# Kernel tuning notes

Hardware: AMD Instinct MI355X
Metric: run time of the kernel (lower is better)

The kernel has to match this reference:

```python
import jax, jax.numpy as jnp
import numpy as np

B, V, N, F = 8, 4, 4096, 256
DV, DA = 64, 128
SF = DV + DA          # slot_full_size = 192
Q = 128               # qry_size
S = 7                 # num_slots
HID = 256             # residual MLP hidden
NUM_STEPS = 3
COEF = 1.0 / np.sqrt(Q).astype(np.float32)
EPS = 1e-5


def _ln(x, g, b):
    m = x.mean(-1, keepdims=True)
    v = ((x - m) ** 2).mean(-1, keepdims=True)
    return (x - m) / jnp.sqrt(v + EPS) * g + b


def _gru(u, h, Wi, Wh, bi, bh):
    gi = u @ Wi + bi
    gh = h @ Wh + bh
    ir, iz, inn = jnp.split(gi, 3, axis=-1)
    hr, hz, hn = jnp.split(gh, 3, axis=-1)
    r = jax.nn.sigmoid(ir + hr)
    z = jax.nn.sigmoid(iz + hz)
    nn_ = jnp.tanh(inn + r * hn)
    return (1.0 - z) * nn_ + z * h


def setup_inputs() -> dict:
    key = jax.random.key(0)
    ks = jax.random.split(key, 12)
    r = lambda k, sh: jax.random.normal(k, sh, jnp.float32) * 0.05
    return {
        'x': jax.random.normal(ks[0], (B, V, N, F), jnp.float32),
        'noise_view': jax.random.normal(ks[1], (B, V, DV), jnp.float32),
        'noise_obj_attr': jax.random.normal(ks[2], (B, S - 1, DA), jnp.float32),
        'noise_bck_attr': jax.random.normal(ks[3], (B, 1, DA), jnp.float32),
        'ln_in_g': jnp.ones((F,), jnp.float32), 'ln_in_b': jnp.zeros((F,), jnp.float32),
        'ln_qry_g': jnp.ones((SF,), jnp.float32), 'ln_qry_b': jnp.zeros((SF,), jnp.float32),
        'ln_res_g': jnp.ones((SF,), jnp.float32), 'ln_res_b': jnp.zeros((SF,), jnp.float32),
        'view_loc': jnp.zeros((DV,), jnp.float32), 'view_log_scl': jnp.zeros((DV,), jnp.float32),
        'attr_obj_loc': jnp.zeros((DA,), jnp.float32), 'attr_obj_scl': jnp.zeros((DA,), jnp.float32),
        'attr_bck_loc': jnp.zeros((DA,), jnp.float32), 'attr_bck_scl': jnp.zeros((DA,), jnp.float32),
        'W_qry': r(ks[4], (SF, Q)), 'W_key': r(ks[5], (F, Q)), 'W_val': r(ks[6], (F, SF)),
        'gru_Wi': r(ks[7], (SF, 3 * SF)), 'gru_Wh': r(ks[8], (SF, 3 * SF)),
        'gru_bi': jnp.zeros((3 * SF,), jnp.float32), 'gru_bh': jnp.zeros((3 * SF,), jnp.float32),
        'mlp_W1': r(ks[9], (SF, HID)), 'mlp_b1': jnp.zeros((HID,), jnp.float32),
        'mlp_W2': r(ks[10], (HID, SF)), 'mlp_b2': jnp.zeros((SF,), jnp.float32),
        'num_slots': S,
    }


def reference(x, noise_view, noise_obj_attr, noise_bck_attr,
              ln_in_g, ln_in_b, ln_qry_g, ln_qry_b, ln_res_g, ln_res_b,
              view_loc, view_log_scl, attr_obj_loc, attr_obj_scl, attr_bck_loc, attr_bck_scl,
              W_qry, W_key, W_val, gru_Wi, gru_Wh, gru_bi, gru_bh,
              mlp_W1, mlp_b1, mlp_W2, mlp_b2, num_slots):
    b, v = x.shape[:2]
    xl = _ln(x, ln_in_g, ln_in_b)
    x_key = xl @ W_key   # [b,v,n,Q]
    x_val = xl @ W_val   # [b,v,n,SF]
    slots_view = view_loc + jnp.exp(view_log_scl) * noise_view                      # [b,v,DV]
    slots_attr = jnp.concatenate([
        attr_obj_loc + jnp.exp(attr_obj_scl) * noise_obj_attr,
        attr_bck_loc + jnp.exp(attr_bck_scl) * noise_bck_attr], axis=1)             # [b,s,DA]
    s = num_slots
    for _ in range(NUM_STEPS):
        full = jnp.concatenate([
            jnp.broadcast_to(slots_view[:, :, None, :], (b, v, s, DV)),
            jnp.broadcast_to(slots_attr[:, None, :, :], (b, v, s, DA))], axis=-1)   # [b,v,s,SF]
        q = _ln(full, ln_qry_g, ln_qry_b) @ W_qry * COEF                            # [b,v,s,Q]
        logits = jnp.einsum('bvni,bvsi->bvns', x_key, q)
        logits = jax.nn.log_softmax(logits, axis=-1)   # over slots
        attn = jax.nn.softmax(logits, axis=-2)         # over inputs
        updates = jnp.einsum('bvns,bvni->bvsi', attn, x_val)                        # [b,v,s,SF]
        main = _gru(updates.reshape(-1, SF), full.reshape(-1, SF),
                    gru_Wi, gru_Wh, gru_bi, gru_bh).reshape(b, v, s, SF)
        res = jax.nn.relu(_ln(main, ln_res_g, ln_res_b) @ mlp_W1 + mlp_b1) @ mlp_W2 + mlp_b2
        full = main + res
        slots_view = full[..., :DV].mean(axis=2)   # mean over slots
        slots_attr = full[..., DV:].mean(axis=1)   # mean over views
    return slots_view, slots_attr
```

## Files before the change

kernel.cpp:

```cpp
#include <hip/hip_runtime.h>
#include <cstdint>
#include <cstddef>

typedef float  f32x4 __attribute__((ext_vector_type(4)));
typedef short  s16x8 __attribute__((ext_vector_type(8)));
typedef __bf16 bf16x8 __attribute__((ext_vector_type(8)));

static __device__ __forceinline__ f32x4 mfma16(s16x8 a, s16x8 b, f32x4 c) {
    return __builtin_amdgcn_mfma_f32_16x16x32_bf16(
        __builtin_bit_cast(bf16x8, a), __builtin_bit_cast(bf16x8, b), c, 0, 0, 0);
}

static __device__ __forceinline__ unsigned short f2bf(float f) {
    unsigned int u = __builtin_bit_cast(unsigned int, f);
    u = (u + 0x7fffu + ((u >> 16) & 1u)) >> 16;
    return (unsigned short)u;
}
static __device__ __forceinline__ float bf2f(unsigned short h) {
    unsigned int u = ((unsigned int)h) << 16;
    return __builtin_bit_cast(float, u);
}

#define COEF 0.08838834764831845f

__global__ __launch_bounds__(256) void k_prep(
    const float* __restrict__ Wkey, const float* __restrict__ Wval,
    const float* __restrict__ vloc, const float* __restrict__ vlscl, const float* __restrict__ nview,
    const float* __restrict__ aoloc, const float* __restrict__ aoscl, const float* __restrict__ nobj,
    const float* __restrict__ abloc, const float* __restrict__ abscl, const float* __restrict__ nbck,
    const float* __restrict__ Wi, const float* __restrict__ Wh,
    const float* __restrict__ W1, const float* __restrict__ W2,
    unsigned short* __restrict__ Wt, unsigned short* __restrict__ qbf,
    float* __restrict__ sview, float* __restrict__ sattr,
    unsigned short* __restrict__ Wib, unsigned short* __restrict__ Whb,
    unsigned short* __restrict__ W1b, unsigned short* __restrict__ W2b)
{
    int blk = blockIdx.x, t = threadIdx.x;
    if (blk < 320) {
        float v = (blk < 128) ? Wkey[t * 128 + blk] : Wval[t * 192 + (blk - 128)];
        Wt[blk * 256 + t] = f2bf(v);
    } else if (blk < 356) {
        int g = (blk - 320) * 256 + t;
        if (g < 2048) {
            int d = g & 63;
            sview[g] = vloc[d] + __expf(vlscl[d]) * nview[g];
        } else {
            int u = g - 2048;
            int b = u / 896, r = u % 896, s = r >> 7, d = r & 127;
            float val;
            if (s < 6) val = aoloc[d] + __expf(aoscl[d]) * nobj[(b * 6 + s) * 128 + d];
            else       val = abloc[d] + __expf(abscl[d]) * nbck[b * 128 + d];
            sattr[u] = val;
        }
    } else if (blk < 360) {
        for (int e = (blk - 356) * 256 + t; e < 32 * 9 * 128; e += 1024) {
            int bv = e / 1152, r = e % 1152, s = 7 + r / 128, k = r & 127;
            qbf[(bv * 16 + s) * 128 + k] = 0;
        }
    } else {
        const float* srcp; unsigned short* dstp; int g4;
        if (blk < 468)      { srcp = Wi; dstp = Wib; g4 = (blk - 360) * 256 + t; }
        else if (blk < 576) { srcp = Wh; dstp = Whb; g4 = (blk - 468) * 256 + t; }
        else if (blk < 624) { srcp = W1; dstp = W1b; g4 = (blk - 576) * 256 + t; }
        else                { srcp = W2; dstp = W2b; g4 = (blk - 624) * 256 + t; }
        float4 v = *(const float4*)(srcp + g4 * 4);
        unsigned u0 = (unsigned)f2bf(v.x) | ((unsigned)f2bf(v.y) << 16);
        unsigned u1 = (unsigned)f2bf(v.z) | ((unsigned)f2bf(v.w) << 16);
        *(uint2*)(dstp + g4 * 4) = make_uint2(u0, u1);
    }
}

__global__ __launch_bounds__(256) void k_lnkv(
    const float* __restrict__ x, const float* __restrict__ lng, const float* __restrict__ lnb,
    const unsigned short* __restrict__ Wt, unsigned short* __restrict__ xkv)
{
    __shared__ unsigned short lds[64 * 320];
    const int t = threadIdx.x, wave = t >> 6, lane = t & 63;
    const int l15 = lane & 15, lg = lane >> 4;
    const long rowbase = (long)blockIdx.x * 64;

    float4 gv = *(const float4*)(lng + lane * 4);
    float4 bv = *(const float4*)(lnb + lane * 4);
    for (int r = 0; r < 16; ++r) {
        int row = wave * 16 + r;
        float4 xv = *(const float4*)(x + (rowbase + row) * 256 + lane * 4);
        float s1 = xv.x + xv.y + xv.z + xv.w;
        float s2 = xv.x * xv.x + xv.y * xv.y + xv.z * xv.z + xv.w * xv.w;
        #pragma unroll
        for (int o = 32; o > 0; o >>= 1) { s1 += __shfl_xor(s1, o); s2 += __shfl_xor(s2, o); }
        float mean = s1 * (1.f / 256.f);
        float var  = s2 * (1.f / 256.f) - mean * mean;
        float rstd = rsqrtf(var + 1e-5f);
        float y0 = (xv.x - mean) * rstd * gv.x + bv.x;
        float y1 = (xv.y - mean) * rstd * gv.y + bv.y;
        float y2 = (xv.z - mean) * rstd * gv.z + bv.z;
        float y3 = (xv.w - mean) * rstd * gv.w + bv.w;
        unsigned int u0 = (unsigned)f2bf(y0) | ((unsigned)f2bf(y1) << 16);
        unsigned int u1 = (unsigned)f2bf(y2) | ((unsigned)f2bf(y3) << 16);
        int off = row * 512 + ((lane * 8) ^ ((row & 7) << 4));
        *(uint2*)((char*)lds + off) = make_uint2(u0, u1);
    }
    __syncthreads();

    f32x4 acc[4][5];
    #pragma unroll
    for (int mt = 0; mt < 4; ++mt)
        #pragma unroll
        for (int nt = 0; nt < 5; ++nt) acc[mt][nt] = (f32x4){0.f, 0.f, 0.f, 0.f};

    const int nb = wave * 80;
    #pragma unroll
    for (int kk = 0; kk < 8; ++kk) {
        s16x8 a[4], b[5];
        #pragma unroll
        for (int mt = 0; mt < 4; ++mt) {
            int row = mt * 16 + l15;
            int off = row * 512 + ((kk * 64 + lg * 16) ^ ((row & 7) << 4));
            a[mt] = *(const s16x8*)((char*)lds + off);
        }
        #pragma unroll
        for (int nt = 0; nt < 5; ++nt) {
            int col = nb + nt * 16 + l15;
            b[nt] = *(const s16x8*)(Wt + col * 256 + kk * 32 + lg * 8);
        }
        #pragma unroll
        for (int mt = 0; mt < 4; ++mt)
            #pragma unroll
            for (int nt = 0; nt < 5; ++nt)
                acc[mt][nt] = mfma16(a[mt], b[nt], acc[mt][nt]);
    }
    __syncthreads();

    #pragma unroll
    for (int mt = 0; mt < 4; ++mt)
        #pragma unroll
        for (int nt = 0; nt < 5; ++nt)
            #pragma unroll
            for (int rg = 0; rg < 4; ++rg) {
                int row = mt * 16 + lg * 4 + rg;
                int col = nb + nt * 16 + l15;
                lds[row * 320 + col] = f2bf(acc[mt][nt][rg]);
            }
    __syncthreads();
    const uint4* src = (const uint4*)lds;
    uint4* dst = (uint4*)(xkv + rowbase * 320);
    #pragma unroll
    for (int j = 0; j < 10; ++j) dst[j * 256 + t] = src[j * 256 + t];
}

__global__ __launch_bounds__(384) void k_qry(
    const float* __restrict__ sview, const float* __restrict__ sattr,
    const float* __restrict__ fnewp, int use_fnew,
    const float* __restrict__ lng, const float* __restrict__ lnb,
    const float* __restrict__ Wq, float* __restrict__ full, unsigned short* __restrict__ qbf)
{
    int row = blockIdx.x;
    int bv = row / 7, s = row % 7, b = bv >> 2;
    int j = threadIdx.x;
    __shared__ float fr[192];
    __shared__ float part[384];
    __shared__ float red[8];
    float v = 0.f;
    if (j < 192) {
        if (use_fnew) {
            if (j < 64) {
                float a = 0.f;
                #pragma unroll
                for (int sp = 0; sp < 7; ++sp) a += fnewp[(bv * 7 + sp) * 192 + j];
                v = a * (1.f / 7.f);
            } else {
                float a = 0.f;
                #pragma unroll
                for (int vv = 0; vv < 4; ++vv) a += fnewp[((b * 4 + vv) * 7 + s) * 192 + j];
                v = a * 0.25f;
            }
        } else {
            v = (j < 64) ? sview[bv * 64 + j] : sattr[(b * 7 + s) * 128 + (j - 64)];
        }
        full[row * 192 + j] = v;
        float s1 = v, s2 = v * v;
        #pragma unroll
        for (int o = 32; o > 0; o >>= 1) { s1 += __shfl_xor(s1, o); s2 += __shfl_xor(s2, o); }
        int wave = j >> 6, lane = j & 63;
        if (lane == 0) { red[wave] = s1; red[4 + wave] = s2; }
    }
    __syncthreads();
    if (j < 192) {
        float ts = red[0] + red[1] + red[2], ts2 = red[4] + red[5] + red[6];
        float mean = ts * (1.f / 192.f);
        float var  = ts2 * (1.f / 192.f) - mean * mean;
        float rstd = rsqrtf(var + 1e-5f);
        fr[j] = (v - mean) * rstd * lng[j] + lnb[j];
    }
    __syncthreads();
    {
        int c = j & 127, seg = j >> 7;
        float acc = 0.f;
        #pragma unroll
        for (int k = 0; k < 64; ++k) acc += fr[seg * 64 + k] * Wq[(seg * 64 + k) * 128 + c];
        part[j] = acc;
    }
    __syncthreads();
    if (j < 128) {
        float acc = part[j] + part[128 + j] + part[256 + j];
        qbf[(bv * 16 + s) * 128 + j] = f2bf(acc * COEF);
    }
}

__global__ __launch_bounds__(256) void k_attu(
    const unsigned short* __restrict__ qbf, const unsigned short* __restrict__ xkv,
    float* __restrict__ pU, float* __restrict__ pZ)
{
    int blk = blockIdx.x;
    int bv = blk >> 5, chunk = blk & 31;
    int n0 = chunk * 128;
    int t = threadIdx.x, wave = t >> 6, lane = t & 63;
    int l15 = lane & 15, lg = lane >> 4;
    __shared__ float wl[128 * 8];

    s16x8 aq[4];
    const unsigned short* qrow = qbf + (bv * 16 + l15) * 128 + lg * 8;
    #pragma unroll
    for (int kk = 0; kk < 4; ++kk) aq[kk] = *(const s16x8*)(qrow + kk * 32);

    #pragma unroll
    for (int batch = 0; batch < 2; ++batch) {
        int nloc = batch * 64 + wave * 16;
        const unsigned short* xr = xkv + ((long)(bv * 4096 + n0 + nloc + l15)) * 320 + lg * 8;
        f32x4 acc = (f32x4){0.f, 0.f, 0.f, 0.f};
        #pragma unroll
        for (int kk = 0; kk < 4; ++kk) {
            s16x8 bfr = *(const s16x8*)(xr + kk * 32);
            acc = mfma16(aq[kk], bfr, acc);
        }
        float o0 = __shfl_xor(acc[0], 16), o1 = __shfl_xor(acc[1], 16);
        float o2 = __shfl_xor(acc[2], 16), o3 = __shfl_xor(acc[3], 16);
        bool hi = (lg & 1);
        float v0 = hi ? o0 : acc[0], v1 = hi ? o1 : acc[1];
        float v2 = hi ? o2 : acc[2], v3 = hi ? o3 : acc[3];
        float v4 = hi ? acc[0] : o0, v5 = hi ? acc[1] : o1, v6 = hi ? acc[2] : o2;
        float m = fmaxf(fmaxf(fmaxf(v0, v1), fmaxf(v2, v3)), fmaxf(fmaxf(v4, v5), v6));
        float e0 = __expf(v0 - m), e1 = __expf(v1 - m), e2 = __expf(v2 - m), e3 = __expf(v3 - m);
        float e4 = __expf(v4 - m), e5 = __expf(v5 - m), e6 = __expf(v6 - m);
        float inv = 1.f / (e0 + e1 + e2 + e3 + e4 + e5 + e6);
        if (lg < 2) {
            int n = nloc + l15;
            float4 out = (lg == 0) ? make_float4(e0 * inv, e1 * inv, e2 * inv, e3 * inv)
                                   : make_float4(e4 * inv, e5 * inv, e6 * inv, 0.f);
            *(float4*)(wl + n * 8 + lg * 4) = out;
        }
    }
    __syncthreads();

    {
        f32x4 uacc[3];
        #pragma unroll
        for (int it = 0; it < 3; ++it) uacc[it] = (f32x4){0.f, 0.f, 0.f, 0.f};
        const unsigned short* vbase = xkv + ((long)(bv * 4096 + n0)) * 320 + 128;

        #pragma unroll
        for (int kb = 0; kb < 4; ++kb) {
            s16x8 aw = (s16x8){0, 0, 0, 0, 0, 0, 0, 0};
            if (l15 < 8) {
                #pragma unroll
                for (int j2 = 0; j2 < 8; ++j2)
                    aw[j2] = (short)f2bf(wl[(kb * 32 + lg * 8 + j2) * 8 + l15]);
            }
            #pragma unroll
            for (int it = 0; it < 3; ++it) {
                int col = wave * 48 + it * 16 + l15;
                s16x8 bw;
                #pragma unroll
                for (int j2 = 0; j2 < 8; ++j2)
                    bw[j2] = (short)vbase[(long)(kb * 32 + lg * 8 + j2) * 320 + col];
                uacc[it] = mfma16(aw, bw, uacc[it]);
            }
        }

        long base = (((long)bv * 32 + chunk) * 7) * 192;
        #pragma unroll
        for (int it = 0; it < 3; ++it) {
            int col = wave * 48 + it * 16 + l15;
            #pragma unroll
            for (int rg = 0; rg < 4; ++rg) {
                int s = lg * 4 + rg;
                if (s < 7) pU[base + s * 192 + col] = uacc[it][rg];
            }
        }
    }

    if (t < 112) {
        int s = t >> 4, part = t & 15;
        float z = 0.f;
        #pragma unroll
        for (int k = 0; k < 8; ++k) z += wl[(part + 16 * k) * 8 + s];
        #pragma unroll
        for (int o = 8; o > 0; o >>= 1) z += __shfl_xor(z, o);
        if (part == 0) pZ[(bv * 32 + chunk) * 7 + s] = z;
    }
}

__global__ __launch_bounds__(576) void k_gru(
    const float* __restrict__ pU, const float* __restrict__ pZ, const float* __restrict__ full,
    const unsigned short* __restrict__ Wib, const unsigned short* __restrict__ Whb,
    const float* __restrict__ bi, const float* __restrict__ bh,
    const float* __restrict__ lng, const float* __restrict__ lnb,
    const unsigned short* __restrict__ W1b, const float* __restrict__ b1,
    const unsigned short* __restrict__ W2b, const float* __restrict__ b2,
    float* __restrict__ fnew)
{
    int row = blockIdx.x;
    int bv = row / 7, s = row % 7;
    int j = threadIdx.x;
    __shared__ float u[192], h[192], gi[576], gh[576], lnm[192], h1[256], red[8];

    if (j < 192) {
        float u0 = 0.f, u1 = 0.f, u2 = 0.f, u3 = 0.f;
        #pragma unroll 4
        for (int c = 0; c < 32; c += 4) {
            u0 += pU[(((long)bv * 32 + c + 0) * 7 + s) * 192 + j];
            u1 += pU[(((long)bv * 32 + c + 1) * 7 + s) * 192 + j];
            u2 += pU[(((long)bv * 32 + c + 2) * 7 + s) * 192 + j];
            u3 += pU[(((long)bv * 32 + c + 3) * 7 + s) * 192 + j];
        }
        float z0 = 0.f, z1 = 0.f, z2 = 0.f, z3 = 0.f;
        #pragma unroll 4
        for (int c = 0; c < 32; c += 4) {
            z0 += pZ[(bv * 32 + c + 0) * 7 + s];
            z1 += pZ[(bv * 32 + c + 1) * 7 + s];
            z2 += pZ[(bv * 32 + c + 2) * 7 + s];
            z3 += pZ[(bv * 32 + c + 3) * 7 + s];
        }
        u[j] = ((u0 + u1) + (u2 + u3)) / ((z0 + z1) + (z2 + z3));
    } else if (j < 384) {
        int jj = j - 192;
        h[jj] = full[row * 192 + jj];
    }
    __syncthreads();

    {
        float a0 = 0.f, a1 = 0.f, a2 = 0.f, a3 = 0.f;
        float b0 = 0.f, b1v = 0.f, b2v = 0.f, b3 = 0.f;
        #pragma unroll 4
        for (int k = 0; k < 192; k += 4) {
            float uk0 = u[k], uk1 = u[k + 1], uk2 = u[k + 2], uk3 = u[k + 3];
            float hk0 = h[k], hk1 = h[k + 1], hk2 = h[k + 2], hk3 = h[k + 3];
            a0  += uk0 * bf2f(Wib[(k + 0) * 576 + j]);
            a1  += uk1 * bf2f(Wib[(k + 1) * 576 + j]);
            a2  += uk2 * bf2f(Wib[(k + 2) * 576 + j]);
            a3  += uk3 * bf2f(Wib[(k + 3) * 576 + j]);
            b0  += hk0 * bf2f(Whb[(k + 0) * 576 + j]);
            b1v += hk1 * bf2f(Whb[(k + 1) * 576 + j]);
            b2v += hk2 * bf2f(Whb[(k + 2) * 576 + j]);
            b3  += hk3 * bf2f(Whb[(k + 3) * 576 + j]);
        }
        gi[j] = ((a0 + a1) + (a2 + a3)) + bi[j];
        gh[j] = ((b0 + b1v) + (b2v + b3)) + bh[j];
    }
    __syncthreads();

    float mn = 0.f;
    if (j < 192) {
        float hv = h[j];
        float r  = 1.f / (1.f + __expf(-(gi[j] + gh[j])));
        float z  = 1.f / (1.f + __expf(-(gi[192 + j] + gh[192 + j])));
        float nn = tanhf(gi[384 + j] + r * gh[384 + j]);
        mn = (1.f - z) * nn + z * hv;

        float s1 = mn, s2 = mn * mn;
        #pragma unroll
        for (int o = 32; o > 0; o >>= 1) { s1 += __shfl_xor(s1, o); s2 += __shfl_xor(s2, o); }
        int wave = j >> 6, lane = j & 63;
        if (lane == 0) { red[wave] = s1; red[4 + wave] = s2; }
    }
    __syncthreads();
    if (j < 192) {
        float ts = red[0] + red[1] + red[2], ts2 = red[4] + red[5] + red[6];
        float mean = ts * (1.f / 192.f);
        float var  = ts2 * (1.f / 192.f) - mean * mean;
        float rstd = rsqrtf(var + 1e-5f);
        lnm[j] = (mn - mean) * rstd * lng[j] + lnb[j];
    }
    __syncthreads();

    if (j < 256) {
        float a0 = 0.f, a1 = 0.f, a2 = 0.f, a3 = 0.f;
        #pragma unroll 4
        for (int k = 0; k < 192; k += 4) {
            a0 += lnm[k + 0] * bf2f(W1b[(k + 0) * 256 + j]);
            a1 += lnm[k + 1] * bf2f(W1b[(k + 1) * 256 + j]);
            a2 += lnm[k + 2] * bf2f(W1b[(k + 2) * 256 + j]);
            a3 += lnm[k + 3] * bf2f(W1b[(k + 3) * 256 + j]);
        }
        h1[j] = fmaxf(((a0 + a1) + (a2 + a3)) + b1[j], 0.f);
    }
    __syncthreads();

    if (j < 192) {
        float a0 = 0.f, a1 = 0.f, a2 = 0.f, a3 = 0.f;
        #pragma unroll 4
        for (int c = 0; c < 256; c += 4) {
            a0 += h1[c + 0] * bf2f(W2b[(c + 0) * 192 + j]);
            a1 += h1[c + 1] * bf2f(W2b[(c + 1) * 192 + j]);
            a2 += h1[c + 2] * bf2f(W2b[(c + 2) * 192 + j]);
            a3 += h1[c + 3] * bf2f(W2b[(c + 3) * 192 + j]);
        }
        fnew[row * 192 + j] = mn + (((a0 + a1) + (a2 + a3)) + b2[j]);
    }
}

__global__ __launch_bounds__(256) void k_means(
    const float* __restrict__ fnew, float* __restrict__ oview, float* __restrict__ oattr)
{
    int t = blockIdx.x * 256 + threadIdx.x;
    if (t < 2048) {
        int bv = t >> 6, d = t & 63;
        float a = 0.f;
        #pragma unroll
        for (int s = 0; s < 7; ++s) a += fnew[(bv * 7 + s) * 192 + d];
        oview[t] = a * (1.f / 7.f);
    } else if (t < 9216) {
        int u = t - 2048;
        int b = u / 896, r = u % 896, s = r >> 7, d = r & 127;
        float a = 0.f;
        #pragma unroll
        for (int v = 0; v < 4; ++v) a += fnew[((b * 4 + v) * 7 + s) * 192 + 64 + d];
        oattr[u] = a * 0.25f;
    }
}

extern "C" void kernel_launch(void* const* d_in, const int* in_sizes, int n_in,
                              void* d_out, int out_size, void* d_ws, size_t ws_size,
                              hipStream_t stream)
{
    const float* x          = (const float*)d_in[0];
    const float* noise_view = (const float*)d_in[1];
    const float* noise_obj  = (const float*)d_in[2];
    const float* noise_bck  = (const float*)d_in[3];
    const float* ln_in_g    = (const float*)d_in[4];
    const float* ln_in_b    = (const float*)d_in[5];
    const float* ln_qry_g   = (const float*)d_in[6];
    const float* ln_qry_b   = (const float*)d_in[7];
    const float* ln_res_g   = (const float*)d_in[8];
    const float* ln_res_b   = (const float*)d_in[9];
    const float* view_loc   = (const float*)d_in[10];
    const float* view_lscl  = (const float*)d_in[11];
    const float* ao_loc     = (const float*)d_in[12];
    const float* ao_scl     = (const float*)d_in[13];
    const float* ab_loc     = (const float*)d_in[14];
    const float* ab_scl     = (const float*)d_in[15];
    const float* W_qry      = (const float*)d_in[16];
    const float* W_key      = (const float*)d_in[17];
    const float* W_val      = (const float*)d_in[18];
    const float* gru_Wi     = (const float*)d_in[19];
    const float* gru_Wh     = (const float*)d_in[20];
    const float* gru_bi     = (const float*)d_in[21];
    const float* gru_bh     = (const float*)d_in[22];
    const float* mlp_W1     = (const float*)d_in[23];
    const float* mlp_b1     = (const float*)d_in[24];
    const float* mlp_W2     = (const float*)d_in[25];
    const float* mlp_b2     = (const float*)d_in[26];

    char* ws = (char*)d_ws;
    size_t off = 0;
    auto alloc = [&](size_t bytes) { void* p = ws + off; off += (bytes + 255) & ~255ULL; return p; };
    unsigned short* xkv = (unsigned short*)alloc(131072UL * 320 * 2);
    unsigned short* Wt  = (unsigned short*)alloc(320UL * 256 * 2);
    unsigned short* qbf = (unsigned short*)alloc(32UL * 16 * 128 * 2);
    float* pU    = (float*)alloc(32UL * 32 * 7 * 192 * 4);
    float* pZ    = (float*)alloc(32UL * 32 * 7 * 4);
    float* fullb = (float*)alloc(224UL * 192 * 4);
    float* fnew  = (float*)alloc(224UL * 192 * 4);
    float* sview = (float*)alloc(2048UL * 4);
    float* sattr = (float*)alloc(7168UL * 4);
    unsigned short* Wib = (unsigned short*)alloc(110592UL * 2);
    unsigned short* Whb = (unsigned short*)alloc(110592UL * 2);
    unsigned short* W1b = (unsigned short*)alloc(49152UL * 2);
    unsigned short* W2b = (unsigned short*)alloc(49152UL * 2);

    k_prep<<<dim3(672), dim3(256), 0, stream>>>(
        W_key, W_val, view_loc, view_lscl, noise_view,
        ao_loc, ao_scl, noise_obj, ab_loc, ab_scl, noise_bck,
        gru_Wi, gru_Wh, mlp_W1, mlp_W2,
        Wt, qbf, sview, sattr, Wib, Whb, W1b, W2b);
    k_lnkv<<<dim3(2048), dim3(256), 0, stream>>>(x, ln_in_g, ln_in_b, Wt, xkv);

    for (int it = 0; it < 3; ++it) {
        k_qry<<<dim3(224), dim3(384), 0, stream>>>(sview, sattr, fnew, (it > 0) ? 1 : 0,
                                                   ln_qry_g, ln_qry_b, W_qry, fullb, qbf);
        k_attu<<<dim3(1024), dim3(256), 0, stream>>>(qbf, xkv, pU, pZ);
        k_gru<<<dim3(224), dim3(576), 0, stream>>>(pU, pZ, fullb, Wib, Whb, gru_bi, gru_bh,
                                                   ln_res_g, ln_res_b, W1b, mlp_b1, W2b, mlp_b2, fnew);
    }
    k_means<<<dim3(36), dim3(256), 0, stream>>>(fnew, (float*)d_out, ((float*)d_out) + 2048);
}
```

Before: 219.9 us.

## Split input layernorm and key/value projection into separate LN and GEMM kernels

Replaces the fused layernorm+projection kernel with two kernels: a high-occupancy LN kernel that writes bf16 normalized rows in a swizzled tile layout to a workspace buffer, and a GEMM kernel that DMAs each tile straight into LDS via global_load_lds before running MFMA. The aim is to spread the latency-bound LN across many small blocks and simplify the GEMM's load path. In exchange it adds a full bf16 round trip of the normalized input through global memory (about 64 MB) and an extra launch, and it falls back to the fused kernel if the workspace is too small.

```diff
diff --git a/kernel.cpp b/kernel.cpp
--- a/kernel.cpp
+++ b/kernel.cpp
@@ -19,6 +19,12 @@
 static __device__ __forceinline__ float bf2f(unsigned short h) {
     unsigned int u = ((unsigned int)h) << 16;
     return __builtin_bit_cast(float, u);
+}
+
+static __device__ __forceinline__ void dma16(const void* g, void* l) {
+    __builtin_amdgcn_global_load_lds(
+        (const __attribute__((address_space(1))) void*)g,
+        (__attribute__((address_space(3))) void*)l, 16, 0, 0);
 }
 
 #define COEF 0.08838834764831845f
@@ -68,6 +74,96 @@
         unsigned u1 = (unsigned)f2bf(v.z) | ((unsigned)f2bf(v.w) << 16);
         *(uint2*)(dstp + g4 * 4) = make_uint2(u0, u1);
     }
+}
+
+__global__ __launch_bounds__(256) void k_ln(
+    const float* __restrict__ x, const float* __restrict__ lng, const float* __restrict__ lnb,
+    unsigned short* __restrict__ xb)
+{
+    const int lane = threadIdx.x & 63;
+    const long row = (long)blockIdx.x * 4 + (threadIdx.x >> 6);
+    float4 xv = *(const float4*)(x + row * 256 + lane * 4);
+    float s1 = xv.x + xv.y + xv.z + xv.w;
+    float s2 = xv.x * xv.x + xv.y * xv.y + xv.z * xv.z + xv.w * xv.w;
+    #pragma unroll
+    for (int o = 32; o > 0; o >>= 1) { s1 += __shfl_xor(s1, o); s2 += __shfl_xor(s2, o); }
+    float mean = s1 * (1.f / 256.f);
+    float var  = s2 * (1.f / 256.f) - mean * mean;
+    float rstd = rsqrtf(var + 1e-5f);
+    float4 gv = *(const float4*)(lng + lane * 4);
+    float4 bv = *(const float4*)(lnb + lane * 4);
+    float y0 = (xv.x - mean) * rstd * gv.x + bv.x;
+    float y1 = (xv.y - mean) * rstd * gv.y + bv.y;
+    float y2 = (xv.z - mean) * rstd * gv.z + bv.z;
+    float y3 = (xv.w - mean) * rstd * gv.w + bv.w;
+    unsigned u0 = (unsigned)f2bf(y0) | ((unsigned)f2bf(y1) << 16);
+    unsigned u1 = (unsigned)f2bf(y2) | ((unsigned)f2bf(y3) << 16);
+    long tile = row >> 6; int lrow = (int)(row & 63);
+    long off = tile * 32768 + (long)(lrow * 512 + ((lane * 8) ^ ((lrow & 7) << 4)));
+    *(uint2*)((char*)xb + off) = make_uint2(u0, u1);
+}
+
+__global__ __launch_bounds__(256) void k_gemm(
+    const unsigned short* __restrict__ xb, const unsigned short* __restrict__ Wt,
+    unsigned short* __restrict__ xkv)
+{
+    __shared__ unsigned short lds[64 * 320];
+    const int t = threadIdx.x, wave = t >> 6, lane = t & 63;
+    const int l15 = lane & 15, lg = lane >> 4;
+    const long rowbase = (long)blockIdx.x * 64;
+
+    const char* src = (const char*)xb + (long)blockIdx.x * 32768;
+    #pragma unroll
+    for (int i = 0; i < 8; ++i) {
+        int off = i * 4096 + t * 16;
+        dma16(src + off, (char*)lds + off);
+    }
+    __syncthreads();
+
+    f32x4 acc[4][5];
+    #pragma unroll
+    for (int mt = 0; mt < 4; ++mt)
+        #pragma unroll
+        for (int nt = 0; nt < 5; ++nt) acc[mt][nt] = (f32x4){0.f, 0.f, 0.f, 0.f};
+
+    const int nb = wave * 80;
+    #pragma unroll
+    for (int kk = 0; kk < 8; ++kk) {
+        s16x8 a[4], b[5];
+        #pragma unroll
+        for (int mt = 0; mt < 4; ++mt) {
+            int row = mt * 16 + l15;
+            int off = row * 512 + ((kk * 64 + lg * 16) ^ ((row & 7) << 4));
+            a[mt] = *(const s16x8*)((char*)lds + off);
+        }
+        #pragma unroll
+        for (int nt = 0; nt < 5; ++nt) {
+            int col = nb + nt * 16 + l15;
+            b[nt] = *(const s16x8*)(Wt + col * 256 + kk * 32 + lg * 8);
+        }
+        #pragma unroll
+        for (int mt = 0; mt < 4; ++mt)
+            #pragma unroll
+            for (int nt = 0; nt < 5; ++nt)
+                acc[mt][nt] = mfma16(a[mt], b[nt], acc[mt][nt]);
+    }
+    __syncthreads();
+
+    #pragma unroll
+    for (int mt = 0; mt < 4; ++mt)
+        #pragma unroll
+        for (int nt = 0; nt < 5; ++nt)
+            #pragma unroll
+            for (int rg = 0; rg < 4; ++rg) {
+                int row = mt * 16 + lg * 4 + rg;
+                int col = nb + nt * 16 + l15;
+                lds[row * 320 + col] = f2bf(acc[mt][nt][rg]);
+            }
+    __syncthreads();
+    const uint4* srcc = (const uint4*)lds;
+    uint4* dst = (uint4*)(xkv + rowbase * 320);
+    #pragma unroll
+    for (int j = 0; j < 10; ++j) dst[j * 256 + t] = srcc[j * 256 + t];
 }
 
 __global__ __launch_bounds__(256) void k_lnkv(
@@ -477,13 +573,20 @@
     unsigned short* Whb = (unsigned short*)alloc(110592UL * 2);
     unsigned short* W1b = (unsigned short*)alloc(49152UL * 2);
     unsigned short* W2b = (unsigned short*)alloc(49152UL * 2);
+    unsigned short* xb  = (unsigned short*)alloc(131072UL * 256 * 2);
+    bool use_split = (off <= ws_size);
 
     k_prep<<<dim3(672), dim3(256), 0, stream>>>(
         W_key, W_val, view_loc, view_lscl, noise_view,
         ao_loc, ao_scl, noise_obj, ab_loc, ab_scl, noise_bck,
         gru_Wi, gru_Wh, mlp_W1, mlp_W2,
         Wt, qbf, sview, sattr, Wib, Whb, W1b, W2b);
-    k_lnkv<<<dim3(2048), dim3(256), 0, stream>>>(x, ln_in_g, ln_in_b, Wt, xkv);
+    if (use_split) {
+        k_ln  <<<dim3(32768), dim3(256), 0, stream>>>(x, ln_in_g, ln_in_b, xb);
+        k_gemm<<<dim3(2048),  dim3(256), 0, stream>>>(xb, Wt, xkv);
+    } else {
+        k_lnkv<<<dim3(2048), dim3(256), 0, stream>>>(x, ln_in_g, ln_in_b, Wt, xkv);
+    }
 
     for (int it = 0; it < 3; ++it) {
         k_qry<<<dim3(224), dim3(384), 0, stream>>>(sview, sattr, fnew, (it > 0) ? 1 : 0,
```

Measured after the change: 242.9 us. 10.5% more time.
